# Performance work log

Hardware: AMD Instinct MI355X
Metric: run time of the kernel (lower is better)

The kernel has to match this reference:

```python
import jax, jax.numpy as jnp
import numpy as np

LIGAND_W = 1.0
SIDECHAIN_W = 0.5
LIGAND_DIST_W = 0.2
SIDECHAIN_DIST_W = 0.1
CUTOFF = 5.0
EPS = 1e-12


def _pdist(x):
    # x: [..., N, 3] -> (dist [..., N, N], sq [..., N, N]); safe sqrt for grads
    d = x[..., :, None, :] - x[..., None, :, :]
    sq = jnp.sum(d * d, axis=-1)
    return jnp.sqrt(jnp.maximum(sq, EPS)), sq


def _masked_dist_loss(pred, tgt, valid):
    # pred/tgt: [..., N, 3], valid: [..., N] float. Returns (per-group loss, has-any flag)
    pd, _ = _pdist(pred)
    td, tsq = _pdist(tgt)
    pair = valid[..., :, None] * valid[..., None, :]
    dmask = pair * (tsq > 0.0).astype(pred.dtype) * (td <= CUTOFF).astype(pred.dtype)
    num = jnp.sum(dmask * (pd - td) ** 2, axis=(-1, -2))
    den = jnp.sum(dmask, axis=(-1, -2))
    return num / jnp.maximum(den, 1.0), den > 0.0


def setup_inputs() -> dict:
    key = jax.random.key(0)
    k1, k2, k3, k4, k5, k6 = jax.random.split(key, 6)
    B, L, R, A = 64, 512, 1024, 14
    ligand_tgt = jax.random.normal(k2, (B, L, 3), dtype=jnp.float32) * 3.0
    ligand_pred = ligand_tgt + 0.5 * jax.random.normal(k1, (B, L, 3), dtype=jnp.float32)
    sidechain_tgt = jax.random.normal(k4, (B, R, A, 3), dtype=jnp.float32) * 2.0
    sidechain_pred = sidechain_tgt + 0.5 * jax.random.normal(k3, (B, R, A, 3), dtype=jnp.float32)
    ligand_mask = jax.random.bernoulli(k5, 0.9, (B, L))
    atom_mask = jax.random.bernoulli(k6, 0.7, (B, R, A))
    return {
        'ligand_pred': ligand_pred, 'ligand_tgt': ligand_tgt,
        'sidechain_pred': sidechain_pred, 'sidechain_tgt': sidechain_tgt,
        'ligand_mask': ligand_mask, 'atom_mask': atom_mask,
    }


def reference(ligand_pred, ligand_tgt, sidechain_pred, sidechain_tgt, ligand_mask, atom_mask):
    f = ligand_pred.dtype
    lm = ligand_mask.astype(f)              # [B, L]
    am = atom_mask.astype(f)                # [B, R, A]

    # --- ligand coord loss: per-batch mse (mean over valid atoms * 3), then mean over batches ---
    se = jnp.sum((ligand_pred - ligand_tgt) ** 2, axis=-1) * lm   # [B, L]
    lig_cnt = jnp.sum(lm, axis=-1)                                # [B]
    ligand_loss = jnp.mean(jnp.sum(se, axis=-1) / (3.0 * jnp.maximum(lig_cnt, 1.0)))

    # --- ligand distance-preservation loss ---
    lig_d, lig_has = _masked_dist_loss(ligand_pred, ligand_tgt, lm)  # [B], [B]
    ligand_dist_loss = jnp.sum(jnp.where(lig_has, lig_d, 0.0)) / jnp.maximum(jnp.sum(lig_has.astype(f)), 1.0)

    # --- sidechain coord loss: per-atom mse (mean over 3), mean over all valid atoms ---
    atom_mse = jnp.mean((sidechain_pred - sidechain_tgt) ** 2, axis=-1)  # [B, R, A]
    sc_cnt = jnp.sum(am)
    sidechain_loss = jnp.sum(atom_mse * am) / jnp.maximum(sc_cnt, 1.0)

    # --- sidechain distance-preservation loss: per-residue groups ---
    sc_d, sc_has = _masked_dist_loss(sidechain_pred, sidechain_tgt, am)  # [B, R]
    sidechain_dist_loss = jnp.sum(jnp.where(sc_has, sc_d, 0.0)) / jnp.maximum(jnp.sum(sc_has.astype(f)), 1.0)

    total = (LIGAND_W * ligand_loss
             + LIGAND_DIST_W * ligand_dist_loss
             + SIDECHAIN_W * sidechain_loss
             + SIDECHAIN_DIST_W * sidechain_dist_loss)
    return total
```

## Files before the change

### kernel.cpp

```cpp
#include <hip/hip_runtime.h>

#define CUTOFF 5.0f
#define DEPS 1e-12f
#define FSQRT(x) __builtin_amdgcn_sqrtf(x)


#define NSC_BLK 512
#define NLIG_BLK 512
#define GRID (NSC_BLK + NLIG_BLK)

#define PAIR_EVAL(ti, pi, tjx, tjy, tjz, pjx, pjy, pjz, w, numv, denv)    \
  {                                                                       \
    float dx = (ti).x - (tjx), dy = (ti).y - (tjy), dz = (ti).z - (tjz);  \
    float tsq = dx * dx + dy * dy + dz * dz;                              \
    float td = FSQRT(fmaxf(tsq, DEPS));                                   \
    float ww = (w);                                                       \
    ww = (tsq > 0.f) ? ww : 0.f;                                          \
    ww = (td <= CUTOFF) ? ww : 0.f;                                       \
    float qx = (pi).x - (pjx), qy = (pi).y - (pjy), qz = (pi).z - (pjz);  \
    float pd = FSQRT(fmaxf(qx * qx + qy * qy + qz * qz, DEPS));           \
    float dd = pd - td;                                                   \
    numv += ww * dd * dd;                                                 \
    denv += ww;                                                           \
  }

__global__ __launch_bounds__(256) void fused_kernel(
    const float* __restrict__ lig_pred, const float* __restrict__ lig_tgt,
    const int* __restrict__ lig_mask,
    const float* __restrict__ sc_pred, const float* __restrict__ sc_tgt,
    const int* __restrict__ sc_mask,
    float* __restrict__ ws) {
  const int tid = threadIdx.x;
  __shared__ float4 stage4[1344];
  __shared__ float red[4][4];

  if (blockIdx.x < NSC_BLK) {
    const int sb = blockIdx.x;
    float ax[7], ay[7], az[7];
    float bx[7], by[7], bz[7];
    float m[7];

    const float4* srcp = (const float4*)(sc_pred + (size_t)sb * 5376);
    for (int k = tid; k < 1344; k += 256) stage4[k] = srcp[k];
    __syncthreads();
    {
      const float* s = ((const float*)stage4) + tid * 21;
#pragma unroll
      for (int a = 0; a < 7; a++) { ax[a] = s[3 * a]; ay[a] = s[3 * a + 1]; az[a] = s[3 * a + 2]; }
    }
    __syncthreads();
    const float4* srct = (const float4*)(sc_tgt + (size_t)sb * 5376);
    for (int k = tid; k < 1344; k += 256) stage4[k] = srct[k];
    __syncthreads();
    {
      const float* s = ((const float*)stage4) + tid * 21;
#pragma unroll
      for (int a = 0; a < 7; a++) { bx[a] = s[3 * a]; by[a] = s[3 * a + 1]; bz[a] = s[3 * a + 2]; }
    }
    const int* mp = sc_mask + (size_t)sb * 1792 + tid * 7;
#pragma unroll
    for (int a = 0; a < 7; a++) m[a] = (mp[a] != 0) ? 1.f : 0.f;

    float mse = 0.f, am = 0.f;
#pragma unroll
    for (int a = 0; a < 7; a++) {
      float dx = ax[a] - bx[a], dy = ay[a] - by[a], dz = az[a] - bz[a];
      mse += m[a] * ((dx * dx + dy * dy + dz * dz) * (1.f / 3.f));
      am += m[a];
    }

    float num = 0.f, den = 0.f;
#pragma unroll
    for (int js = 0; js < 7; js++) {
#pragma unroll
      for (int side = 0; side < 2; side++) {
        float jx, jy, jz, kx, ky, kz, mj;
        if (side == 0) {
          jx = ax[js]; jy = ay[js]; jz = az[js];
          kx = bx[js]; ky = by[js]; kz = bz[js];
          mj = m[js];
        } else {
          jx = __shfl_xor(ax[js], 1, 64); jy = __shfl_xor(ay[js], 1, 64);
          jz = __shfl_xor(az[js], 1, 64);
          kx = __shfl_xor(bx[js], 1, 64); ky = __shfl_xor(by[js], 1, 64);
          kz = __shfl_xor(bz[js], 1, 64);
          mj = __shfl_xor(m[js], 1, 64);
        }
#pragma unroll
        for (int i = 0; i < 7; i++) {
          float dx = bx[i] - kx, dy = by[i] - ky, dz = bz[i] - kz;
          float tsq = dx * dx + dy * dy + dz * dz;
          float td = FSQRT(fmaxf(tsq, DEPS));
          float w = m[i] * mj;
          w = (tsq > 0.f) ? w : 0.f;
          w = (td <= CUTOFF) ? w : 0.f;
          float qx = ax[i] - jx, qy = ay[i] - jy, qz = az[i] - jz;
          float pd = FSQRT(fmaxf(qx * qx + qy * qy + qz * qz, DEPS));
          float d = pd - td;
          num += w * d * d;
          den += w;
        }
      }
    }
    float num_g = num + __shfl_xor(num, 1, 64);
    float den_g = den + __shfl_xor(den, 1, 64);
    float val = (den_g > 0.f) ? 0.5f * (num_g / fmaxf(den_g, 1.f)) : 0.f;
    float has = (den_g > 0.f) ? 0.5f : 0.f;

    for (int off = 32; off > 0; off >>= 1) {
      mse += __shfl_down(mse, off, 64);
      am += __shfl_down(am, off, 64);
      val += __shfl_down(val, off, 64);
      has += __shfl_down(has, off, 64);
    }
    int lane = tid & 63, wv = tid >> 6;
    if (lane == 0) { red[0][wv] = mse; red[1][wv] = am; red[2][wv] = val; red[3][wv] = has; }
    __syncthreads();
    if (tid == 0) {
      float* p = ws + 1088 + (size_t)sb * 4;
      p[0] = red[0][0] + red[0][1] + red[0][2] + red[0][3];
      p[1] = red[1][0] + red[1][1] + red[1][2] + red[1][3];
      p[2] = red[2][0] + red[2][1] + red[2][2] + red[2][3];
      p[3] = red[3][0] + red[3][1] + red[3][2] + red[3][3];
    }
  } else {
    const int L = 512;
    const int lb = blockIdx.x - NSC_BLK;
    const int b = lb >> 3;
    const int t = lb & 7;
    const int i0a = 32 * t;
    const int i0b = 32 * (15 - t);
    const float* pb = lig_pred + (size_t)b * L * 3;
    const float* tb = lig_tgt + (size_t)b * L * 3;
    const int* mb = lig_mask + (size_t)b * L;

    float4* st4 = stage4;
    float4* sp4 = stage4 + 64;

    if (tid < 128) {
      int which = tid >> 5;
      int idx = tid & 31;
      int i = ((which & 1) ? i0b : i0a) + idx;
      if (which < 2) {
        st4[(which << 5) + idx] =
            make_float4(tb[3 * i], tb[3 * i + 1], tb[3 * i + 2], (mb[i] != 0) ? 1.f : 0.f);
      } else {
        sp4[((which & 1) << 5) + idx] =
            make_float4(pb[3 * i], pb[3 * i + 1], pb[3 * i + 2], 0.f);
      }
    }

    const int jA0 = i0a + tid;
    const int jA1r = i0a + 256 + tid;
    const int jA1 = jA1r & (L - 1);
    const int jBr = i0b + tid;
    const int jB = jBr & (L - 1);

    float pA0x = pb[3 * jA0], pA0y = pb[3 * jA0 + 1], pA0z = pb[3 * jA0 + 2];
    float tA0x = tb[3 * jA0], tA0y = tb[3 * jA0 + 1], tA0z = tb[3 * jA0 + 2];
    float mA0 = (mb[jA0] != 0) ? 1.f : 0.f;
    float pA1x = pb[3 * jA1], pA1y = pb[3 * jA1 + 1], pA1z = pb[3 * jA1 + 2];
    float tA1x = tb[3 * jA1], tA1y = tb[3 * jA1 + 1], tA1z = tb[3 * jA1 + 2];
    float mA1 = (jA1r < L && mb[jA1] != 0) ? 1.f : 0.f;
    float pBx = pb[3 * jB], pBy = pb[3 * jB + 1], pBz = pb[3 * jB + 2];
    float tBx = tb[3 * jB], tBy = tb[3 * jB + 1], tBz = tb[3 * jB + 2];
    float mB = (jBr < L && mb[jB] != 0) ? 1.f : 0.f;

    float se = 0.f, cnt = 0.f;
    if (t == 0) {
      float dx = pA0x - tA0x, dy = pA0y - tA0y, dz = pA0z - tA0z;
      se += mA0 * (dx * dx + dy * dy + dz * dz);
      cnt += mA0;
      dx = pA1x - tA1x; dy = pA1y - tA1y; dz = pA1z - tA1z;
      se += mA1 * (dx * dx + dy * dy + dz * dz);
      cnt += mA1;
    }
    __syncthreads();

    float nA0 = 0.f, dA0 = 0.f, nA1 = 0.f, dA1 = 0.f, nB = 0.f, dB = 0.f;
#pragma unroll 8
    for (int ii = 0; ii < 32; ii++) {
      float4 tiA = st4[ii];
      float4 piA = sp4[ii];
      float4 tiB = st4[32 + ii];
      float4 piB = sp4[32 + ii];
      float wA0 = (tid > ii) ? tiA.w * mA0 : 0.f;
      PAIR_EVAL(tiA, piA, tA0x, tA0y, tA0z, pA0x, pA0y, pA0z, wA0, nA0, dA0);
      float wA1 = tiA.w * mA1;
      PAIR_EVAL(tiA, piA, tA1x, tA1y, tA1z, pA1x, pA1y, pA1z, wA1, nA1, dA1);
      float wB = (tid > ii) ? tiB.w * mB : 0.f;
      PAIR_EVAL(tiB, piB, tBx, tBy, tBz, pBx, pBy, pBz, wB, nB, dB);
    }

    float num = nA0 + nA1 + nB, den = dA0 + dA1 + dB;
    for (int off = 32; off > 0; off >>= 1) {
      num += __shfl_down(num, off, 64);
      den += __shfl_down(den, off, 64);
      se += __shfl_down(se, off, 64);
      cnt += __shfl_down(cnt, off, 64);
    }
    int lane = tid & 63, wv = tid >> 6;
    if (lane == 0) { red[0][wv] = num; red[1][wv] = den; red[2][wv] = se; red[3][wv] = cnt; }
    __syncthreads();
    if (tid == 0) {
      ws[lb * 2 + 0] = red[0][0] + red[0][1] + red[0][2] + red[0][3];
      ws[lb * 2 + 1] = red[1][0] + red[1][1] + red[1][2] + red[1][3];
      if (t == 0) {
        float se_t = red[2][0] + red[2][1] + red[2][2] + red[2][3];
        float cnt_t = red[3][0] + red[3][1] + red[3][2] + red[3][3];
        ws[1024 + b] = se_t / (3.f * fmaxf(cnt_t, 1.f));
      }
    }
  }
}

__global__ __launch_bounds__(256) void finalize_kernel(const float* __restrict__ ws,
                                                       float* __restrict__ out) {
  const int tid = threadIdx.x;
  __shared__ float sred[4][4];

  const float* sc = ws + 1088;
  float s0 = 0.f, s1 = 0.f, s2 = 0.f, s3 = 0.f;
  for (int i = tid; i < 512; i += 256) {
    s0 += sc[4 * i + 0]; s1 += sc[4 * i + 1]; s2 += sc[4 * i + 2]; s3 += sc[4 * i + 3];
  }
  for (int off = 32; off > 0; off >>= 1) {
    s0 += __shfl_down(s0, off, 64);
    s1 += __shfl_down(s1, off, 64);
    s2 += __shfl_down(s2, off, 64);
    s3 += __shfl_down(s3, off, 64);
  }
  int lane = tid & 63, wv = tid >> 6;
  if (lane == 0) { sred[0][wv] = s0; sred[1][wv] = s1; sred[2][wv] = s2; sred[3][wv] = s3; }
  __syncthreads();

  float lval = 0.f, lhas = 0.f, lcoord = 0.f;
  if (tid < 64) {
    float n = 0.f, d = 0.f;
    for (int t = 0; t < 8; t++) {
      n += ws[(tid * 8 + t) * 2 + 0];
      d += ws[(tid * 8 + t) * 2 + 1];
    }
    lval = (d > 0.f) ? n / fmaxf(d, 1.f) : 0.f;
    lhas = (d > 0.f) ? 1.f : 0.f;
    lcoord = ws[1024 + tid];
    for (int off = 32; off > 0; off >>= 1) {
      lval += __shfl_down(lval, off, 64);
      lhas += __shfl_down(lhas, off, 64);
      lcoord += __shfl_down(lcoord, off, 64);
    }
  }
  if (tid == 0) {
    float sc_mse = sred[0][0] + sred[0][1] + sred[0][2] + sred[0][3];
    float sc_am = sred[1][0] + sred[1][1] + sred[1][2] + sred[1][3];
    float sc_val = sred[2][0] + sred[2][1] + sred[2][2] + sred[2][3];
    float sc_has = sred[3][0] + sred[3][1] + sred[3][2] + sred[3][3];
    float ligand_loss = lcoord * (1.f / 64.f);
    float ligand_dist_loss = lval / fmaxf(lhas, 1.f);
    float sidechain_loss = sc_mse / fmaxf(sc_am, 1.f);
    float sidechain_dist_loss = sc_val / fmaxf(sc_has, 1.f);
    out[0] = ligand_loss + 0.2f * ligand_dist_loss + 0.5f * sidechain_loss +
             0.1f * sidechain_dist_loss;
  }
}

extern "C" void kernel_launch(void* const* d_in, const int* in_sizes, int n_in,
                              void* d_out, int out_size, void* d_ws, size_t ws_size,
                              hipStream_t stream) {
  const float* ligand_pred = (const float*)d_in[0];
  const float* ligand_tgt = (const float*)d_in[1];
  const float* sidechain_pred = (const float*)d_in[2];
  const float* sidechain_tgt = (const float*)d_in[3];
  const int* ligand_mask = (const int*)d_in[4];
  const int* atom_mask = (const int*)d_in[5];
  float* out = (float*)d_out;
  float* ws = (float*)d_ws;

  fused_kernel<<<GRID, 256, 0, stream>>>(ligand_pred, ligand_tgt, ligand_mask,
                                         sidechain_pred, sidechain_tgt, atom_mask, ws);
  finalize_kernel<<<1, 256, 0, stream>>>(ws, out);
}
```

Measured before the change: 105.1 us.

## Split ligand pair blocks in two and add occupancy hint with split accumulators

Each ligand block's three pair streams are split across two blocks: one handles the triangular A0 stream and the other handles the A1 and B streams. This doubles the ligand grid to raise parallelism and shorten per-block latency. The sidechain and ligand loops gain dual accumulators to break the add dependency chains, and launch_bounds now requests 5 blocks per CU. The coord-loss partials are now written per half and combined in finalize, which changes the workspace layout. The work per block is uneven (one stream versus two) and the extra blocks add staging overhead.

```diff
diff --git a/kernel.cpp b/kernel.cpp
--- a/kernel.cpp
+++ b/kernel.cpp
@@ -6,7 +6,7 @@
 
 
 #define NSC_BLK 512
-#define NLIG_BLK 512
+#define NLIG_BLK 1024
 #define GRID (NSC_BLK + NLIG_BLK)
 
 #define PAIR_EVAL(ti, pi, tjx, tjy, tjz, pjx, pjy, pjz, w, numv, denv)    \
@@ -24,7 +24,7 @@
     denv += ww;                                                           \
   }
 
-__global__ __launch_bounds__(256) void fused_kernel(
+__global__ __launch_bounds__(256, 5) void fused_kernel(
     const float* __restrict__ lig_pred, const float* __restrict__ lig_tgt,
     const int* __restrict__ lig_mask,
     const float* __restrict__ sc_pred, const float* __restrict__ sc_tgt,
@@ -69,7 +69,7 @@
       am += m[a];
     }
 
-    float num = 0.f, den = 0.f;
+    float num0 = 0.f, den0 = 0.f, num1 = 0.f, den1 = 0.f;
 #pragma unroll
     for (int js = 0; js < 7; js++) {
 #pragma unroll
@@ -97,11 +97,12 @@
           float qx = ax[i] - jx, qy = ay[i] - jy, qz = az[i] - jz;
           float pd = FSQRT(fmaxf(qx * qx + qy * qy + qz * qz, DEPS));
           float d = pd - td;
-          num += w * d * d;
-          den += w;
+          if (i & 1) { num1 += w * d * d; den1 += w; }
+          else       { num0 += w * d * d; den0 += w; }
         }
       }
     }
+    float num = num0 + num1, den = den0 + den1;
     float num_g = num + __shfl_xor(num, 1, 64);
     float den_g = den + __shfl_xor(den, 1, 64);
     float val = (den_g > 0.f) ? 0.5f * (num_g / fmaxf(den_g, 1.f)) : 0.f;
@@ -117,7 +118,7 @@
     if (lane == 0) { red[0][wv] = mse; red[1][wv] = am; red[2][wv] = val; red[3][wv] = has; }
     __syncthreads();
     if (tid == 0) {
-      float* p = ws + 1088 + (size_t)sb * 4;
+      float* p = ws + 2304 + (size_t)sb * 4;
       p[0] = red[0][0] + red[0][1] + red[0][2] + red[0][3];
       p[1] = red[1][0] + red[1][1] + red[1][2] + red[1][3];
       p[2] = red[2][0] + red[2][1] + red[2][2] + red[2][3];
@@ -126,8 +127,10 @@
   } else {
     const int L = 512;
     const int lb = blockIdx.x - NSC_BLK;
-    const int b = lb >> 3;
-    const int t = lb & 7;
+    const int b = lb >> 4;
+    const int sub = lb & 15;
+    const int t = sub >> 1;
+    const int half = sub & 1;
     const int i0a = 32 * t;
     const int i0b = 32 * (15 - t);
     const float* pb = lig_pred + (size_t)b * L * 3;
@@ -137,62 +140,84 @@
     float4* st4 = stage4;
     float4* sp4 = stage4 + 64;
 
-    if (tid < 128) {
-      int which = tid >> 5;
-      int idx = tid & 31;
-      int i = ((which & 1) ? i0b : i0a) + idx;
-      if (which < 2) {
-        st4[(which << 5) + idx] =
-            make_float4(tb[3 * i], tb[3 * i + 1], tb[3 * i + 2], (mb[i] != 0) ? 1.f : 0.f);
-      } else {
-        sp4[((which & 1) << 5) + idx] =
-            make_float4(pb[3 * i], pb[3 * i + 1], pb[3 * i + 2], 0.f);
-      }
-    }
-
-    const int jA0 = i0a + tid;
-    const int jA1r = i0a + 256 + tid;
-    const int jA1 = jA1r & (L - 1);
-    const int jBr = i0b + tid;
-    const int jB = jBr & (L - 1);
-
-    float pA0x = pb[3 * jA0], pA0y = pb[3 * jA0 + 1], pA0z = pb[3 * jA0 + 2];
-    float tA0x = tb[3 * jA0], tA0y = tb[3 * jA0 + 1], tA0z = tb[3 * jA0 + 2];
-    float mA0 = (mb[jA0] != 0) ? 1.f : 0.f;
-    float pA1x = pb[3 * jA1], pA1y = pb[3 * jA1 + 1], pA1z = pb[3 * jA1 + 2];
-    float tA1x = tb[3 * jA1], tA1y = tb[3 * jA1 + 1], tA1z = tb[3 * jA1 + 2];
-    float mA1 = (jA1r < L && mb[jA1] != 0) ? 1.f : 0.f;
-    float pBx = pb[3 * jB], pBy = pb[3 * jB + 1], pBz = pb[3 * jB + 2];
-    float tBx = tb[3 * jB], tBy = tb[3 * jB + 1], tBz = tb[3 * jB + 2];
-    float mB = (jBr < L && mb[jB] != 0) ? 1.f : 0.f;
-
-    float se = 0.f, cnt = 0.f;
-    if (t == 0) {
-      float dx = pA0x - tA0x, dy = pA0y - tA0y, dz = pA0z - tA0z;
-      se += mA0 * (dx * dx + dy * dy + dz * dz);
-      cnt += mA0;
-      dx = pA1x - tA1x; dy = pA1y - tA1y; dz = pA1z - tA1z;
-      se += mA1 * (dx * dx + dy * dy + dz * dz);
-      cnt += mA1;
-    }
-    __syncthreads();
-
-    float nA0 = 0.f, dA0 = 0.f, nA1 = 0.f, dA1 = 0.f, nB = 0.f, dB = 0.f;
+    if (half == 0) {
+      if (tid < 32) {
+        int i = i0a + tid;
+        st4[tid] = make_float4(tb[3 * i], tb[3 * i + 1], tb[3 * i + 2], (mb[i] != 0) ? 1.f : 0.f);
+      } else if (tid < 64) {
+        int i = i0a + tid - 32;
+        sp4[tid - 32] = make_float4(pb[3 * i], pb[3 * i + 1], pb[3 * i + 2], 0.f);
+      }
+    } else {
+      if (tid < 128) {
+        int which = tid >> 5;
+        int idx = tid & 31;
+        int i = ((which & 1) ? i0b : i0a) + idx;
+        if (which < 2) {
+          st4[(which << 5) + idx] =
+              make_float4(tb[3 * i], tb[3 * i + 1], tb[3 * i + 2], (mb[i] != 0) ? 1.f : 0.f);
+        } else {
+          sp4[((which & 1) << 5) + idx] =
+              make_float4(pb[3 * i], pb[3 * i + 1], pb[3 * i + 2], 0.f);
+        }
+      }
+    }
+
+    float num = 0.f, den = 0.f, se = 0.f, cnt = 0.f;
+
+    if (half == 0) {
+      const int jA0 = i0a + tid;
+      float pjx = pb[3 * jA0], pjy = pb[3 * jA0 + 1], pjz = pb[3 * jA0 + 2];
+      float tjx = tb[3 * jA0], tjy = tb[3 * jA0 + 1], tjz = tb[3 * jA0 + 2];
+      float mj = (mb[jA0] != 0) ? 1.f : 0.f;
+      if (t == 0) {
+        float dx = pjx - tjx, dy = pjy - tjy, dz = pjz - tjz;
+        se += mj * (dx * dx + dy * dy + dz * dz);
+        cnt += mj;
+      }
+      __syncthreads();
+      float n0 = 0.f, d0 = 0.f, n1 = 0.f, d1 = 0.f;
 #pragma unroll 8
-    for (int ii = 0; ii < 32; ii++) {
-      float4 tiA = st4[ii];
-      float4 piA = sp4[ii];
-      float4 tiB = st4[32 + ii];
-      float4 piB = sp4[32 + ii];
-      float wA0 = (tid > ii) ? tiA.w * mA0 : 0.f;
-      PAIR_EVAL(tiA, piA, tA0x, tA0y, tA0z, pA0x, pA0y, pA0z, wA0, nA0, dA0);
-      float wA1 = tiA.w * mA1;
-      PAIR_EVAL(tiA, piA, tA1x, tA1y, tA1z, pA1x, pA1y, pA1z, wA1, nA1, dA1);
-      float wB = (tid > ii) ? tiB.w * mB : 0.f;
-      PAIR_EVAL(tiB, piB, tBx, tBy, tBz, pBx, pBy, pBz, wB, nB, dB);
-    }
-
-    float num = nA0 + nA1 + nB, den = dA0 + dA1 + dB;
+      for (int ii = 0; ii < 32; ii++) {
+        float4 ti = st4[ii];
+        float4 pi = sp4[ii];
+        float w = (tid > ii) ? ti.w * mj : 0.f;
+        if (ii & 1) { PAIR_EVAL(ti, pi, tjx, tjy, tjz, pjx, pjy, pjz, w, n1, d1); }
+        else        { PAIR_EVAL(ti, pi, tjx, tjy, tjz, pjx, pjy, pjz, w, n0, d0); }
+      }
+      num = n0 + n1; den = d0 + d1;
+    } else {
+      const int jA1r = i0a + 256 + tid;
+      const int jA1 = jA1r & (L - 1);
+      const int jBr = i0b + tid;
+      const int jB = jBr & (L - 1);
+      float pA1x = pb[3 * jA1], pA1y = pb[3 * jA1 + 1], pA1z = pb[3 * jA1 + 2];
+      float tA1x = tb[3 * jA1], tA1y = tb[3 * jA1 + 1], tA1z = tb[3 * jA1 + 2];
+      float mA1 = (jA1r < L && mb[jA1] != 0) ? 1.f : 0.f;
+      float pBx = pb[3 * jB], pBy = pb[3 * jB + 1], pBz = pb[3 * jB + 2];
+      float tBx = tb[3 * jB], tBy = tb[3 * jB + 1], tBz = tb[3 * jB + 2];
+      float mB = (jBr < L && mb[jB] != 0) ? 1.f : 0.f;
+      if (t == 0) {
+        float dx = pA1x - tA1x, dy = pA1y - tA1y, dz = pA1z - tA1z;
+        se += mA1 * (dx * dx + dy * dy + dz * dz);
+        cnt += mA1;
+      }
+      __syncthreads();
+      float nA1 = 0.f, dA1 = 0.f, nB = 0.f, dB = 0.f;
+#pragma unroll 8
+      for (int ii = 0; ii < 32; ii++) {
+        float4 tiA = st4[ii];
+        float4 piA = sp4[ii];
+        float4 tiB = st4[32 + ii];
+        float4 piB = sp4[32 + ii];
+        float wA1 = tiA.w * mA1;
+        PAIR_EVAL(tiA, piA, tA1x, tA1y, tA1z, pA1x, pA1y, pA1z, wA1, nA1, dA1);
+        float wB = (tid > ii) ? tiB.w * mB : 0.f;
+        PAIR_EVAL(tiB, piB, tBx, tBy, tBz, pBx, pBy, pBz, wB, nB, dB);
+      }
+      num = nA1 + nB; den = dA1 + dB;
+    }
+
     for (int off = 32; off > 0; off >>= 1) {
       num += __shfl_down(num, off, 64);
       den += __shfl_down(den, off, 64);
@@ -206,9 +231,9 @@
       ws[lb * 2 + 0] = red[0][0] + red[0][1] + red[0][2] + red[0][3];
       ws[lb * 2 + 1] = red[1][0] + red[1][1] + red[1][2] + red[1][3];
       if (t == 0) {
-        float se_t = red[2][0] + red[2][1] + red[2][2] + red[2][3];
-        float cnt_t = red[3][0] + red[3][1] + red[3][2] + red[3][3];
-        ws[1024 + b] = se_t / (3.f * fmaxf(cnt_t, 1.f));
+        float* c = ws + 2048 + (size_t)b * 4 + half * 2;
+        c[0] = red[2][0] + red[2][1] + red[2][2] + red[2][3];
+        c[1] = red[3][0] + red[3][1] + red[3][2] + red[3][3];
       }
     }
   }
@@ -219,7 +244,7 @@
   const int tid = threadIdx.x;
   __shared__ float sred[4][4];
 
-  const float* sc = ws + 1088;
+  const float* sc = ws + 2304;
   float s0 = 0.f, s1 = 0.f, s2 = 0.f, s3 = 0.f;
   for (int i = tid; i < 512; i += 256) {
     s0 += sc[4 * i + 0]; s1 += sc[4 * i + 1]; s2 += sc[4 * i + 2]; s3 += sc[4 * i + 3];
@@ -237,13 +262,15 @@
   float lval = 0.f, lhas = 0.f, lcoord = 0.f;
   if (tid < 64) {
     float n = 0.f, d = 0.f;
-    for (int t = 0; t < 8; t++) {
-      n += ws[(tid * 8 + t) * 2 + 0];
-      d += ws[(tid * 8 + t) * 2 + 1];
+    for (int s = 0; s < 16; s++) {
+      n += ws[(tid * 16 + s) * 2 + 0];
+      d += ws[(tid * 16 + s) * 2 + 1];
     }
     lval = (d > 0.f) ? n / fmaxf(d, 1.f) : 0.f;
     lhas = (d > 0.f) ? 1.f : 0.f;
-    lcoord = ws[1024 + tid];
+    float se = ws[2048 + tid * 4 + 0] + ws[2048 + tid * 4 + 2];
+    float cnt = ws[2048 + tid * 4 + 1] + ws[2048 + tid * 4 + 3];
+    lcoord = se / (3.f * fmaxf(cnt, 1.f));
     for (int off = 32; off > 0; off >>= 1) {
       lval += __shfl_down(lval, off, 64);
       lhas += __shfl_down(lhas, off, 64);
```

After: 117.5 us. 11.8% more time.
